# Optimization experiments

Measured on AMD Instinct MI355X. Metric: run time of the kernel, lower is better.

The kernel has to match this reference:

```python
import jax, jax.numpy as jnp
import numpy as np

B, P, T = 64, 8400, 100


def _corners(b):
    # b: [..., 4] in (cx, cy, w, h) -> (x1, y1, x2, y2)
    cx, cy, w, h = b[..., 0], b[..., 1], b[..., 2], b[..., 3]
    return cx - w / 2, cy - h / 2, cx + w / 2, cy + h / 2


def _pairwise_iou(pred_box, tgt_box):
    # pred_box: [B, P, 4], tgt_box: [B, T, 4] -> iou [B, T, P]
    px1, py1, px2, py2 = _corners(pred_box[:, None, :, :])   # [B,1,P]
    tx1, ty1, tx2, ty2 = _corners(tgt_box[:, :, None, :])    # [B,T,1]
    ix1 = jnp.maximum(px1, tx1)
    iy1 = jnp.maximum(py1, ty1)
    ix2 = jnp.minimum(px2, tx2)
    iy2 = jnp.minimum(py2, ty2)
    inter = jnp.maximum(ix2 - ix1, 0.0) * jnp.maximum(iy2 - iy1, 0.0)
    area_p = (px2 - px1) * (py2 - py1)
    area_t = (tx2 - tx1) * (ty2 - ty1)
    return inter / (area_p + area_t - inter + 1e-6)


def setup_inputs() -> dict:
    key = jax.random.key(0)
    k1, k2, k3 = jax.random.split(key, 3)
    predictions = jax.random.uniform(k1, (B, P, 5), dtype=jnp.float32)
    targets = jax.random.uniform(k2, (B, T, 5), dtype=jnp.float32)
    lengths = jax.random.randint(k3, (B,), 0, T, dtype=jnp.int64)
    return {"predictions": predictions, "targets": targets, "lengths": lengths}


def reference(predictions, targets, lengths):
    # predictions: [B, P, 5], targets: [B, T, 5], lengths: [B]
    iou = _pairwise_iou(predictions[..., 1:], targets[..., 1:])  # [B, T, P]
    # strict '>' in original keeps first max; argmax also returns first occurrence
    best_idx = jnp.argmax(iou, axis=-1)                          # [B, T]
    matched = jnp.take_along_axis(predictions, best_idx[..., None], axis=1)  # [B, T, 5]
    sq = jnp.sum((matched - targets) ** 2, axis=-1)              # [B, T]
    valid = jnp.arange(targets.shape[1]) < lengths[:, None]      # [B, T]
    loss = jnp.sum(jnp.where(valid, sq, 0.0)) / predictions.shape[0]
    return loss
```

## Files before the change

kernel.cpp:

```cpp
#include <hip/hip_runtime.h>

#define BB 64
#define PP 8400
#define TT 100

__global__ __launch_bounds__(256) void yolo_match_kernel(
    const float* __restrict__ pred,
    const float* __restrict__ tgt,
    const int*   __restrict__ lengths,
    float* __restrict__ ws)
{
#pragma clang fp contract(off)
    const int bt  = blockIdx.x;
    const int b   = bt / TT;
    const int t   = bt - b * TT;
    const int tid = threadIdx.x;

    const float* pb = pred + (size_t)b * PP * 5;
    const float* tb = tgt  + ((size_t)b * TT + t) * 5;

    const float tcx = tb[1], tcy = tb[2], tw = tb[3], th = tb[4];
    const float tx1 = tcx - tw * 0.5f;
    const float ty1 = tcy - th * 0.5f;
    const float tx2 = tcx + tw * 0.5f;
    const float ty2 = tcy + th * 0.5f;
    const float area_t = (tx2 - tx1) * (ty2 - ty1);

    float best = -1.0f;
    int   bidx = 0;

    for (int p = tid; p < PP; p += 256) {
        const float* bp = pb + p * 5;
        const float cx = bp[1], cy = bp[2], w = bp[3], h = bp[4];
        const float px1 = cx - w * 0.5f;
        const float py1 = cy - h * 0.5f;
        const float px2 = cx + w * 0.5f;
        const float py2 = cy + h * 0.5f;

        const float ix1 = fmaxf(px1, tx1);
        const float iy1 = fmaxf(py1, ty1);
        const float ix2 = fminf(px2, tx2);
        const float iy2 = fminf(py2, ty2);

        const float inter  = fmaxf(ix2 - ix1, 0.0f) * fmaxf(iy2 - iy1, 0.0f);
        const float area_p = (px2 - px1) * (py2 - py1);
        const float denom = ((area_p + area_t) - inter) + 1e-6f;
        const float iou   = inter / denom;

        if (iou > best) { best = iou; bidx = p; }
    }

    __shared__ float s_iou[256];
    __shared__ int   s_idx[256];
    s_iou[tid] = best;
    s_idx[tid] = bidx;
    __syncthreads();

    for (int off = 128; off > 0; off >>= 1) {
        if (tid < off) {
            const float o  = s_iou[tid + off];
            const int   oi = s_idx[tid + off];
            const float m  = s_iou[tid];
            const int   mi = s_idx[tid];
            if (o > m || (o == m && oi < mi)) {
                s_iou[tid] = o;
                s_idx[tid] = oi;
            }
        }
        __syncthreads();
    }

    if (tid == 0) {
        const int bi = s_idx[0];
        const float* mp = pb + bi * 5;
        float sq = 0.0f;
        for (int k = 0; k < 5; ++k) {
            const float d = mp[k] - tb[k];
            sq += d * d;
        }
        const bool valid = (t < lengths[b]);
        ws[bt] = valid ? sq : 0.0f;
    }
}

__global__ __launch_bounds__(256) void yolo_reduce_kernel(
    const float* __restrict__ ws,
    float* __restrict__ out)
{
    const int tid = threadIdx.x;
    float s = 0.0f;
    for (int i = tid; i < BB * TT; i += 256) s += ws[i];

    __shared__ float sm[256];
    sm[tid] = s;
    __syncthreads();
    for (int off = 128; off > 0; off >>= 1) {
        if (tid < off) sm[tid] += sm[tid + off];
        __syncthreads();
    }
    if (tid == 0) out[0] = sm[0] / (float)BB;
}

extern "C" void kernel_launch(void* const* d_in, const int* in_sizes, int n_in,
                              void* d_out, int out_size, void* d_ws, size_t ws_size,
                              hipStream_t stream) {
    const float* pred    = (const float*)d_in[0];
    const float* tgt     = (const float*)d_in[1];
    const int*   lengths = (const int*)d_in[2];
    float* out = (float*)d_out;
    float* ws  = (float*)d_ws;

    yolo_match_kernel<<<BB * TT, 256, 0, stream>>>(pred, tgt, lengths, ws);
    yolo_reduce_kernel<<<1, 256, 0, stream>>>(ws, out);
}
```

Before: 120.6 us.

## Process ten targets per block to reuse prediction loads, use wave shuffles

Each block now handles a group of 10 targets for one batch, so every prediction box loaded from memory is reused across 10 IoU computations held in registers. The shared-memory tree reduction is replaced by wavefront shuffle reductions per target, followed by a small cross-wave merge. The grid shrinks from 6400 to 640 blocks, which cuts redundant global loads but reduces parallelism and raises register pressure.

```diff
diff --git a/kernel.cpp b/kernel.cpp
--- a/kernel.cpp
+++ b/kernel.cpp
@@ -3,6 +3,8 @@
 #define BB 64
 #define PP 8400
 #define TT 100
+#define TG 10
+#define NGRP (TT / TG)
 
 __global__ __launch_bounds__(256) void yolo_match_kernel(
     const float* __restrict__ pred,
@@ -11,23 +13,31 @@
     float* __restrict__ ws)
 {
 #pragma clang fp contract(off)
-    const int bt  = blockIdx.x;
-    const int b   = bt / TT;
-    const int t   = bt - b * TT;
+    const int blk = blockIdx.x;
+    const int b   = blk / NGRP;
+    const int grp = blk - b * NGRP;
+    const int t0  = grp * TG;
     const int tid = threadIdx.x;
 
     const float* pb = pred + (size_t)b * PP * 5;
-    const float* tb = tgt  + ((size_t)b * TT + t) * 5;
+    const float* tb = tgt  + ((size_t)b * TT + t0) * 5;
 
-    const float tcx = tb[1], tcy = tb[2], tw = tb[3], th = tb[4];
-    const float tx1 = tcx - tw * 0.5f;
-    const float ty1 = tcy - th * 0.5f;
-    const float tx2 = tcx + tw * 0.5f;
-    const float ty2 = tcy + th * 0.5f;
-    const float area_t = (tx2 - tx1) * (ty2 - ty1);
+    float tx1[TG], ty1[TG], tx2[TG], ty2[TG], ta[TG];
+#pragma unroll
+    for (int g = 0; g < TG; ++g) {
+        const float tcx = tb[g * 5 + 1], tcy = tb[g * 5 + 2];
+        const float tw  = tb[g * 5 + 3], th  = tb[g * 5 + 4];
+        tx1[g] = tcx - tw * 0.5f;
+        ty1[g] = tcy - th * 0.5f;
+        tx2[g] = tcx + tw * 0.5f;
+        ty2[g] = tcy + th * 0.5f;
+        ta[g]  = (tx2[g] - tx1[g]) * (ty2[g] - ty1[g]);
+    }
 
-    float best = -1.0f;
-    int   bidx = 0;
+    float best[TG];
+    int   bidx[TG];
+#pragma unroll
+    for (int g = 0; g < TG; ++g) { best[g] = -1.0f; bidx[g] = 0; }
 
     for (int p = tid; p < PP; p += 256) {
         const float* bp = pb + p * 5;
@@ -36,50 +46,67 @@
         const float py1 = cy - h * 0.5f;
         const float px2 = cx + w * 0.5f;
         const float py2 = cy + h * 0.5f;
+        const float area_p = (px2 - px1) * (py2 - py1);
 
-        const float ix1 = fmaxf(px1, tx1);
-        const float iy1 = fmaxf(py1, ty1);
-        const float ix2 = fminf(px2, tx2);
-        const float iy2 = fminf(py2, ty2);
-
-        const float inter  = fmaxf(ix2 - ix1, 0.0f) * fmaxf(iy2 - iy1, 0.0f);
-        const float area_p = (px2 - px1) * (py2 - py1);
-        const float denom = ((area_p + area_t) - inter) + 1e-6f;
-        const float iou   = inter / denom;
-
-        if (iou > best) { best = iou; bidx = p; }
+#pragma unroll
+        for (int g = 0; g < TG; ++g) {
+            const float ix1 = fmaxf(px1, tx1[g]);
+            const float iy1 = fmaxf(py1, ty1[g]);
+            const float ix2 = fminf(px2, tx2[g]);
+            const float iy2 = fminf(py2, ty2[g]);
+            const float inter = fmaxf(ix2 - ix1, 0.0f) * fmaxf(iy2 - iy1, 0.0f);
+            const float denom = ((area_p + ta[g]) - inter) + 1e-6f;
+            const float iou   = inter / denom;
+            if (iou > best[g]) { best[g] = iou; bidx[g] = p; }
+        }
     }
 
-    __shared__ float s_iou[256];
-    __shared__ int   s_idx[256];
-    s_iou[tid] = best;
-    s_idx[tid] = bidx;
+    const int lane = tid & 63;
+    const int wid  = tid >> 6;
+    __shared__ float s_best[4][TG];
+    __shared__ int   s_bidx[4][TG];
+    __shared__ float s_sq[TG];
+
+#pragma unroll
+    for (int g = 0; g < TG; ++g) {
+        float bv = best[g];
+        int   bi = bidx[g];
+        for (int off = 32; off > 0; off >>= 1) {
+            const float ob = __shfl_down(bv, off, 64);
+            const int   oi = __shfl_down(bi, off, 64);
+            if (ob > bv || (ob == bv && oi < bi)) { bv = ob; bi = oi; }
+        }
+        if (lane == 0) { s_best[wid][g] = bv; s_bidx[wid][g] = bi; }
+    }
     __syncthreads();
 
-    for (int off = 128; off > 0; off >>= 1) {
-        if (tid < off) {
-            const float o  = s_iou[tid + off];
-            const int   oi = s_idx[tid + off];
-            const float m  = s_iou[tid];
-            const int   mi = s_idx[tid];
-            if (o > m || (o == m && oi < mi)) {
-                s_iou[tid] = o;
-                s_idx[tid] = oi;
-            }
+    if (tid < TG) {
+        const int g = tid;
+        float bv = s_best[0][g];
+        int   bi = s_bidx[0][g];
+#pragma unroll
+        for (int w = 1; w < 4; ++w) {
+            const float ob = s_best[w][g];
+            const int   oi = s_bidx[w][g];
+            if (ob > bv || (ob == bv && oi < bi)) { bv = ob; bi = oi; }
         }
-        __syncthreads();
+        const float* mp = pb + bi * 5;
+        const float* tp = tb + g * 5;
+        float sq = 0.0f;
+        for (int k = 0; k < 5; ++k) {
+            const float d = mp[k] - tp[k];
+            sq += d * d;
+        }
+        const bool valid = ((t0 + g) < lengths[b]);
+        s_sq[g] = valid ? sq : 0.0f;
     }
+    __syncthreads();
 
     if (tid == 0) {
-        const int bi = s_idx[0];
-        const float* mp = pb + bi * 5;
-        float sq = 0.0f;
-        for (int k = 0; k < 5; ++k) {
-            const float d = mp[k] - tb[k];
-            sq += d * d;
-        }
-        const bool valid = (t < lengths[b]);
-        ws[bt] = valid ? sq : 0.0f;
+        float s = 0.0f;
+#pragma unroll
+        for (int g = 0; g < TG; ++g) s += s_sq[g];
+        ws[blk] = s;
     }
 }
 
@@ -89,7 +116,7 @@
 {
     const int tid = threadIdx.x;
     float s = 0.0f;
-    for (int i = tid; i < BB * TT; i += 256) s += ws[i];
+    for (int i = tid; i < BB * NGRP; i += 256) s += ws[i];
 
     __shared__ float sm[256];
     sm[tid] = s;
@@ -110,6 +137,6 @@
     float* out = (float*)d_out;
     float* ws  = (float*)d_ws;
 
-    yolo_match_kernel<<<BB * TT, 256, 0, stream>>>(pred, tgt, lengths, ws);
+    yolo_match_kernel<<<BB * NGRP, 256, 0, stream>>>(pred, tgt, lengths, ws);
     yolo_reduce_kernel<<<1, 256, 0, stream>>>(ws, out);
 }
```

New measurement: 121.0 us. Within noise of the previous version (+0.3%).
